# Optimization experiments

Measured on AMD Instinct MI355X. Metric: run time of the kernel, lower is better.

The kernel has to match this reference:

```python
import jax, jax.numpy as jnp
import numpy as np

IN_DIM, OUT_DIM, ATTN_DIM, N_REL = 128, 128, 64, 200
N_NODE, N_EDGE, N_QUERY = 50000, 500000, 64
VOCAB = 2 * N_REL + 1  # 401


def setup_inputs() -> dict:
    key = jax.random.key(0)
    ks = jax.random.split(key, 16)
    # edge table [E,7]: col0=r_idx, col2=rel, col4=sub, col5=obj, col6=time; cols 1,3 unused
    e = np.zeros((N_EDGE, 7), dtype=np.int64)
    e[:, 0] = np.asarray(jax.random.randint(ks[0], (N_EDGE,), 0, N_QUERY))
    e[:, 2] = np.asarray(jax.random.randint(ks[1], (N_EDGE,), 0, VOCAB))
    e[:, 4] = np.asarray(jax.random.randint(ks[2], (N_EDGE,), 0, N_NODE))
    e[:, 5] = np.asarray(jax.random.randint(ks[3], (N_EDGE,), 0, N_NODE))
    e[:, 6] = np.asarray(jax.random.randint(ks[4], (N_EDGE,), 0, 1000))
    s = 0.05
    return {
        "q_sub": jax.random.randint(ks[5], (N_QUERY,), 0, N_NODE),
        "q_rel": jax.random.randint(ks[6], (N_QUERY,), 0, VOCAB),
        "hidden": jax.random.normal(ks[7], (N_NODE, IN_DIM), jnp.float32),
        "edges": jnp.asarray(e),
        "n_node": N_NODE,
        "rela_embed": jax.random.normal(ks[8], (VOCAB, IN_DIM), jnp.float32),
        "Ws_W": jax.random.normal(ks[9], (ATTN_DIM, IN_DIM), jnp.float32) * s,
        "Wr_W": jax.random.normal(ks[10], (ATTN_DIM, IN_DIM), jnp.float32) * s,
        "Wqr_W": jax.random.normal(ks[11], (ATTN_DIM, IN_DIM), jnp.float32) * s,
        "Wqr_b": jnp.zeros((ATTN_DIM,), jnp.float32),
        "walpha_W": jax.random.normal(ks[12], (1, ATTN_DIM), jnp.float32) * s,
        "gateW_W": jax.random.normal(ks[13], (2 * IN_DIM, 3 * IN_DIM), jnp.float32) * s,
        "gateW_b": jnp.zeros((2 * IN_DIM,), jnp.float32),
        "ht_W": jax.random.normal(ks[14], (IN_DIM, 2 * IN_DIM), jnp.float32) * s,
        "ht_b": jnp.zeros((IN_DIM,), jnp.float32),
        "Wh_W": jax.random.normal(ks[15], (OUT_DIM, IN_DIM), jnp.float32) * s,
    }


def reference(q_sub, q_rel, hidden, edges, n_node, rela_embed,
              Ws_W, Wr_W, Wqr_W, Wqr_b, walpha_W,
              gateW_W, gateW_b, ht_W, ht_b, Wh_W):
    sub, rel, obj, r_idx = edges[:, 4], edges[:, 2], edges[:, 5], edges[:, 0]
    # unique+inverse on (rel,time) then embedding of rel == direct embedding lookup
    hr = rela_embed[rel]              # [E, in]
    hs = hidden[sub]                  # [E, in]
    h_qr = rela_embed[q_rel][r_idx]   # [E, in]
    # GateUnit(message=hr, factor=h_qr, hidden_state=hs)
    factors = jnp.concatenate([hr, h_qr, hs], axis=1)
    gates = jax.nn.sigmoid(factors @ gateW_W.T + gateW_b)
    update, reset = jnp.split(gates, 2, axis=1)
    cand = jnp.tanh(jnp.concatenate([hr, reset * hs], axis=1) @ ht_W.T + ht_b)
    message = (1.0 - update) * hs + update * cand
    # attention score
    pre = hs @ Ws_W.T + hr @ Wr_W.T + (h_qr @ Wqr_W.T + Wqr_b)
    alpha = jax.nn.leaky_relu(pre, 0.01) @ walpha_W.T  # [E,1]
    up_message = jax.nn.sigmoid(alpha) * message
    # scatter-sum over destination nodes + sqrt-degree normalization
    agg = jax.ops.segment_sum(up_message, obj, num_segments=n_node)
    deg = jax.ops.segment_sum(jnp.ones((up_message.shape[0], 1), jnp.float32), obj, num_segments=n_node)
    agg = agg / jnp.sqrt(deg + 0.0001)
    return agg @ Wh_W.T  # act = identity
```

## Files before the change

kernel.cpp:

```cpp
#include <hip/hip_runtime.h>

typedef unsigned short ushort_t;
typedef __attribute__((ext_vector_type(8))) short short8;
typedef __attribute__((ext_vector_type(4))) float f32x4;

#define DEV __device__ __forceinline__

DEV float sigm(float x) { return 1.0f / (1.0f + __expf(-x)); }
DEV float tanh_fast(float x) { return 1.0f - 2.0f / (__expf(2.0f * x) + 1.0f); }
DEV ushort_t f2bf(float v) {
    unsigned u = __float_as_uint(v);
    unsigned r = (u + 0x7fffu + ((u >> 16) & 1u)) >> 16;
    return (ushort_t)r;
}
DEV float bf2f(ushort_t h) { return __uint_as_float(((unsigned)h) << 16); }
DEV unsigned cvt_pk(float lo, float hi) {
    unsigned r;
    asm("v_cvt_pk_bf16_f32 %0, %1, %2" : "=v"(r) : "v"(lo), "v"(hi));
    return r;
}
DEV float dot4(float4 a, float4 b) {
    return fmaf(a.x, b.x, fmaf(a.y, b.y, fmaf(a.z, b.z, a.w * b.w)));
}

__global__ __launch_bounds__(256) void hist_kernel(
    const int* __restrict__ edges, int nEdge, int* __restrict__ cnt)
{
    int i = blockIdx.x * 256 + threadIdx.x;
    if (i < nEdge) atomicAdd(cnt + edges[(size_t)i * 7 + 5], 1);
}

__global__ __launch_bounds__(256) void scan1_kernel(
    const int* __restrict__ cnt, int n, int* __restrict__ partials)
{
    __shared__ int s[256];
    int t = threadIdx.x;
    int i = blockIdx.x * 256 + t;
    s[t] = (i < n) ? cnt[i] : 0;
    __syncthreads();
    for (int o = 128; o > 0; o >>= 1) {
        if (t < o) s[t] += s[t + o];
        __syncthreads();
    }
    if (t == 0) partials[blockIdx.x] = s[0];
}

__global__ __launch_bounds__(256) void scan2_kernel(
    const int* __restrict__ cnt, int n, const int* __restrict__ partials,
    int nBlk, int* __restrict__ start, int* __restrict__ cursor)
{
    __shared__ int ps[256];
    __shared__ int loc[256];
    int t = threadIdx.x, b = blockIdx.x;
    ps[t] = (t < nBlk) ? partials[t] : 0;
    __syncthreads();
    for (int o = 1; o < 256; o <<= 1) {
        int v = (t >= o) ? ps[t - o] : 0;
        __syncthreads();
        ps[t] += v;
        __syncthreads();
    }
    int offset = (b > 0) ? ps[b - 1] : 0;
    int i = b * 256 + t;
    int v = (i < n) ? cnt[i] : 0;
    loc[t] = v;
    __syncthreads();
    for (int o = 1; o < 256; o <<= 1) {
        int x = (t >= o) ? loc[t - o] : 0;
        __syncthreads();
        loc[t] += x;
        __syncthreads();
    }
    if (i < n) {
        int excl = offset + loc[t] - v;
        start[i] = excl;
        cursor[i] = excl;
    }
}

__global__ __launch_bounds__(256) void build_kernel(
    const int* __restrict__ edges, int nEdge, int* __restrict__ cursor,
    int4* __restrict__ sorted)
{
    int i = blockIdx.x * 256 + threadIdx.x;
    if (i < nEdge) {
        const int* er = edges + (size_t)i * 7;
        int obj = er[5];
        int s = atomicAdd(cursor + obj, 1);
        sorted[s] = make_int4(er[0], er[2], er[4], obj);
    }
}

__global__ __launch_bounds__(256) void table_kernel(
    const float* __restrict__ rela, const int* __restrict__ q_rel,
    const float* __restrict__ gateW, const float* __restrict__ gateW_b,
    const float* __restrict__ WrW, const float* __restrict__ WqrW,
    const float* __restrict__ Wqr_b, const float* __restrict__ htW,
    const float* __restrict__ ht_b,
    float* __restrict__ grhr, float* __restrict__ gq,
    float* __restrict__ whr, float* __restrict__ wq,
    float* __restrict__ thr, int vocab)
{
    __shared__ float x[128];
    int b = blockIdx.x, t = threadIdx.x;
    bool isRel = b < vocab;
    int src = isRel ? b : q_rel[b - vocab];
    if (t < 128) x[t] = rela[src * 128 + t];
    __syncthreads();
    const float4* x4 = (const float4*)x;
    {
        const float4* wrow = (const float4*)(gateW + t * 384 + (isRel ? 0 : 128));
        float acc = isRel ? 0.0f : gateW_b[t];
#pragma unroll 8
        for (int i = 0; i < 32; i++) acc += dot4(wrow[i], x4[i]);
        float* dst = isRel ? (grhr + b * 256) : (gq + (b - vocab) * 256);
        dst[2 * (t & 127) + (t >> 7)] = acc;
    }
    if (isRel) {
        if (t < 192) {
            bool isWr = t < 64;
            int i = isWr ? t : (t - 64);
            const float4* wrow = (const float4*)(isWr ? (WrW + i * 128) : (htW + i * 256));
            float acc = isWr ? 0.0f : ht_b[i];
#pragma unroll 8
            for (int q = 0; q < 32; q++) acc += dot4(wrow[q], x4[q]);
            if (isWr) whr[b * 64 + i] = acc;
            else      thr[b * 128 + i] = acc;
        }
    } else {
        if (t < 64) {
            const float4* wrow = (const float4*)(WqrW + t * 128);
            float acc = Wqr_b[t];
#pragma unroll 8
            for (int q = 0; q < 32; q++) acc += dot4(wrow[q], x4[q]);
            wq[(b - vocab) * 64 + t] = acc;
        }
    }
}

__global__ __launch_bounds__(256) void node_kernel(
    const float* __restrict__ hidden, const float* __restrict__ gateW,
    const float* __restrict__ WsW,
    ushort_t* __restrict__ gate_hs, ushort_t* __restrict__ ws_hs,
    ushort_t* __restrict__ hsb, int nNode)
{
    __shared__ char a_lds[32 * 256];
    int t = threadIdx.x, w = t >> 6, l = t & 63;
    int lm = l & 15, lh = l >> 4;
    int nbase = blockIdx.x * 32;

    for (int idx = t; idx < 1024; idx += 256) {
        int row = idx >> 5, c4 = idx & 31;
        int node = nbase + row;
        float4 v = (node < nNode) ? ((const float4*)hidden)[(size_t)node * 32 + c4]
                                  : float4{0.f, 0.f, 0.f, 0.f};
        uint2 p;
        p.x = cvt_pk(v.x, v.y);
        p.y = cvt_pk(v.z, v.w);
        *(uint2*)(a_lds + ((row * 256 + c4 * 8) ^ ((row & 7) << 4))) = p;
        if (node < nNode) *(uint2*)(hsb + (size_t)node * 128 + c4 * 4) = p;
    }

    short8 bfr[5][4];
#pragma unroll
    for (int nt = 0; nt < 5; nt++)
#pragma unroll
        for (int kt = 0; kt < 4; kt++) {
            int row = w * 80 + nt * 16 + lm;
            const float* src = (row < 256)
                ? gateW + (size_t)row * 384 + 256 + kt * 32 + lh * 8
                : WsW + (size_t)(row - 256) * 128 + kt * 32 + lh * 8;
            float4 f0 = *(const float4*)src;
            float4 f1 = *(const float4*)(src + 4);
            union { unsigned u[4]; short8 s; } tmp;
            tmp.u[0] = cvt_pk(f0.x, f0.y); tmp.u[1] = cvt_pk(f0.z, f0.w);
            tmp.u[2] = cvt_pk(f1.x, f1.y); tmp.u[3] = cvt_pk(f1.z, f1.w);
            bfr[nt][kt] = tmp.s;
        }
    __syncthreads();

    short8 afr[2][4];
#pragma unroll
    for (int mt = 0; mt < 2; mt++)
#pragma unroll
        for (int kt = 0; kt < 4; kt++) {
            int row = mt * 16 + lm;
            afr[mt][kt] = *(const short8*)(a_lds +
                ((row * 256 + kt * 64 + lh * 16) ^ ((row & 7) << 4)));
        }
    f32x4 acc[2][5];
#pragma unroll
    for (int mt = 0; mt < 2; mt++)
#pragma unroll
        for (int nt = 0; nt < 5; nt++) acc[mt][nt] = (f32x4){0.f, 0.f, 0.f, 0.f};
#pragma unroll
    for (int kt = 0; kt < 4; kt++)
#pragma unroll
        for (int mt = 0; mt < 2; mt++)
#pragma unroll
            for (int nt = 0; nt < 5; nt++)
                acc[mt][nt] = __builtin_amdgcn_mfma_f32_16x16x32_bf16(
                    afr[mt][kt], bfr[nt][kt], acc[mt][nt], 0, 0, 0);

#pragma unroll
    for (int mt = 0; mt < 2; mt++)
#pragma unroll
        for (int nt = 0; nt < 5; nt++) {
            int wrow = w * 80 + nt * 16 + lm;
#pragma unroll
            for (int r = 0; r < 4; r++) {
                int node = nbase + mt * 16 + lh * 4 + r;
                if (node < nNode) {
                    ushort_t v = f2bf(acc[mt][nt][r]);
                    if (wrow < 256)
                        gate_hs[(size_t)node * 256 + 2 * (wrow & 127) + (wrow >> 7)] = v;
                    else
                        ws_hs[(size_t)node * 64 + wrow - 256] = v;
                }
            }
        }
}

__global__ __launch_bounds__(256, 6) void edge_kernel(
    const int4* __restrict__ sorted, int nEdge,
    const float* __restrict__ grhr, const float* __restrict__ gq,
    const float* __restrict__ whr, const float* __restrict__ wq,
    const float* __restrict__ thr,
    const ushort_t* __restrict__ gate_hs, const ushort_t* __restrict__ ws_hs,
    const ushort_t* __restrict__ hsb,
    const float* __restrict__ walpha, const float* __restrict__ htW,
    float* __restrict__ agg)
{
    __shared__ ushort_t xb[32 * 128];
    __shared__ unsigned ab[32 * 128];
    __shared__ int4 eds4[32];

    int t = threadIdx.x, w = t >> 6, l = t & 63;
    int lm = l & 15, lh = l >> 4;
    int n0 = w * 32;

    int nb = gridDim.x;
    int xcd = blockIdx.x & 7, lid = blockIdx.x >> 3;
    int q = nb >> 3, rr = nb & 7;
    int sbid = ((xcd < rr) ? xcd * (q + 1) : rr * (q + 1) + (xcd - rr) * q) + lid;
    int ebase = sbid * 32;

    if (t < 32) {
        int gi = ebase + t;
        eds4[t] = (gi < nEdge) ? sorted[gi] : make_int4(0, 0, 0, -1);
    }

    short8 bfr[2][4];
#pragma unroll
    for (int nt = 0; nt < 2; nt++)
#pragma unroll
        for (int kt = 0; kt < 4; kt++) {
            const float* src = htW + (size_t)(n0 + nt * 16 + lm) * 256 + 128 + kt * 32 + lh * 8;
            float4 f0 = *(const float4*)src;
            float4 f1 = *(const float4*)(src + 4);
            union { unsigned u[4]; short8 s; } tmp;
            tmp.u[0] = cvt_pk(f0.x, f0.y); tmp.u[1] = cvt_pk(f0.z, f0.w);
            tmp.u[2] = cvt_pk(f1.x, f1.y); tmp.u[3] = cvt_pk(f1.z, f1.w);
            bfr[nt][kt] = tmp.s;
        }
    float wal = walpha[l];
    __syncthreads();

#pragma unroll 4
    for (int i = 0; i < 8; i++) {
        int e = w * 8 + i;
        int4 er = eds4[e];
        int ridx = er.x, rel = er.y, sub = er.z;
        ushort4 gp = *(const ushort4*)(gate_hs + (size_t)sub * 256 + 4 * l);
        float4 ga = *(const float4*)(grhr + (size_t)rel * 256 + 4 * l);
        float4 gb = *(const float4*)(gq + (size_t)ridx * 256 + 4 * l);
        unsigned hp = *(const unsigned*)(hsb + (size_t)sub * 128 + 2 * l);
        float h0 = bf2f((ushort_t)(hp & 0xffffu));
        float h1 = bf2f((ushort_t)(hp >> 16));
        float u0 = sigm(ga.x + gb.x + bf2f(gp.x));
        float r0 = sigm(ga.y + gb.y + bf2f(gp.y));
        float u1 = sigm(ga.z + gb.z + bf2f(gp.z));
        float r1 = sigm(ga.w + gb.w + bf2f(gp.w));
        float aa = bf2f(ws_hs[(size_t)sub * 64 + l]) + whr[rel * 64 + l] + wq[ridx * 64 + l];
        aa = (aa > 0.0f) ? aa : 0.01f * aa;
        float v = aa * wal;
#pragma unroll
        for (int o = 32; o > 0; o >>= 1) v += __shfl_xor(v, o, 64);
        float sga = sigm(v);
        unsigned xw = cvt_pk(r0 * h0, r1 * h1);
        *(unsigned*)((char*)xb + ((e * 256 + 4 * l) ^ ((e & 7) << 4))) = xw;
        float A0 = sga * (1.0f - u0) * h0;
        float A1 = sga * (1.0f - u1) * h1;
        uint2 abp;
        abp.x = cvt_pk(A0, sga * u0);
        abp.y = cvt_pk(A1, sga * u1);
        *(uint2*)((char*)ab + ((e * 512 + 8 * l) ^ (((e >> 2) & 3) << 6))) = abp;
    }
    __syncthreads();

    short8 afr[2][4];
#pragma unroll
    for (int mt = 0; mt < 2; mt++)
#pragma unroll
        for (int kt = 0; kt < 4; kt++) {
            int e = mt * 16 + lm;
            afr[mt][kt] = *(const short8*)((const char*)xb +
                ((e * 256 + kt * 64 + lh * 16) ^ ((e & 7) << 4)));
        }
    f32x4 acc[2][2];
#pragma unroll
    for (int mt = 0; mt < 2; mt++)
#pragma unroll
        for (int nt = 0; nt < 2; nt++) acc[mt][nt] = (f32x4){0.f, 0.f, 0.f, 0.f};
#pragma unroll
    for (int kt = 0; kt < 4; kt++)
#pragma unroll
        for (int mt = 0; mt < 2; mt++)
#pragma unroll
            for (int nt = 0; nt < 2; nt++)
                acc[mt][nt] = __builtin_amdgcn_mfma_f32_16x16x32_bf16(
                    afr[mt][kt], bfr[nt][kt], acc[mt][nt], 0, 0, 0);

#pragma unroll
    for (int mt = 0; mt < 2; mt++)
#pragma unroll
        for (int nt = 0; nt < 2; nt++) {
            int d = n0 + nt * 16 + lm;
            float vals[4];
            int objs[4];
#pragma unroll
            for (int r = 0; r < 4; r++) {
                int e = mt * 16 + lh * 4 + r;
                int rel = eds4[e].y;
                objs[r] = eds4[e].w;
                float th = thr[rel * 128 + d];
                float cand = tanh_fast(acc[mt][nt][r] + th);
                unsigned abw = *(const unsigned*)((const char*)ab +
                    ((e * 512 + 4 * d) ^ (((e >> 2) & 3) << 6)));
                vals[r] = bf2f((ushort_t)(abw & 0xffffu)) +
                          bf2f((ushort_t)(abw >> 16)) * cand;
            }
            float sum = vals[0];
            int prev = objs[0];
#pragma unroll
            for (int r = 1; r < 4; r++) {
                if (objs[r] == prev) {
                    sum += vals[r];
                } else {
                    if (prev >= 0) atomicAdd(agg + (size_t)prev * 128 + d, sum);
                    sum = vals[r];
                    prev = objs[r];
                }
            }
            if (prev >= 0) atomicAdd(agg + (size_t)prev * 128 + d, sum);
        }
}

__global__ __launch_bounds__(256) void final_kernel(
    const float* __restrict__ WhW, const int* __restrict__ degi,
    float* __restrict__ agg, int nNode)
{
    __shared__ char y_lds[64 * 256];
    int t = threadIdx.x, w = t >> 6, l = t & 63;
    int lm = l & 15, lh = l >> 4;
    int nbase = blockIdx.x * 64;

    short8 bfr[2][4];
#pragma unroll
    for (int nt = 0; nt < 2; nt++)
#pragma unroll
        for (int kt = 0; kt < 4; kt++) {
            const float* src = WhW + (size_t)(w * 32 + nt * 16 + lm) * 128 + kt * 32 + lh * 8;
            float4 f0 = *(const float4*)src;
            float4 f1 = *(const float4*)(src + 4);
            union { unsigned u[4]; short8 s; } tmp;
            tmp.u[0] = cvt_pk(f0.x, f0.y); tmp.u[1] = cvt_pk(f0.z, f0.w);
            tmp.u[2] = cvt_pk(f1.x, f1.y); tmp.u[3] = cvt_pk(f1.z, f1.w);
            bfr[nt][kt] = tmp.s;
        }

    for (int idx = t; idx < 2048; idx += 256) {
        int row = idx >> 5, c4 = idx & 31;
        int node = nbase + row;
        uint2 p = {0u, 0u};
        if (node < nNode) {
            float4 v = ((const float4*)agg)[(size_t)node * 32 + c4];
            float r = 1.0f / sqrtf((float)degi[node] + 1e-4f);
            p.x = cvt_pk(v.x * r, v.y * r);
            p.y = cvt_pk(v.z * r, v.w * r);
        }
        *(uint2*)(y_lds + ((row * 256 + c4 * 8) ^ ((row & 7) << 4))) = p;
    }
    __syncthreads();

    short8 afr[4][4];
#pragma unroll
    for (int mt = 0; mt < 4; mt++)
#pragma unroll
        for (int kt = 0; kt < 4; kt++) {
            int row = mt * 16 + lm;
            afr[mt][kt] = *(const short8*)(y_lds +
                ((row * 256 + kt * 64 + lh * 16) ^ ((row & 7) << 4)));
        }
    f32x4 acc[4][2];
#pragma unroll
    for (int mt = 0; mt < 4; mt++)
#pragma unroll
        for (int nt = 0; nt < 2; nt++) acc[mt][nt] = (f32x4){0.f, 0.f, 0.f, 0.f};
#pragma unroll
    for (int kt = 0; kt < 4; kt++)
#pragma unroll
        for (int mt = 0; mt < 4; mt++)
#pragma unroll
            for (int nt = 0; nt < 2; nt++)
                acc[mt][nt] = __builtin_amdgcn_mfma_f32_16x16x32_bf16(
                    afr[mt][kt], bfr[nt][kt], acc[mt][nt], 0, 0, 0);

#pragma unroll
    for (int mt = 0; mt < 4; mt++)
#pragma unroll
        for (int nt = 0; nt < 2; nt++) {
            int col = w * 32 + nt * 16 + lm;
#pragma unroll
            for (int r = 0; r < 4; r++) {
                int node = nbase + mt * 16 + lh * 4 + r;
                if (node < nNode) agg[(size_t)node * 128 + col] = acc[mt][nt][r];
            }
        }
}

extern "C" void kernel_launch(void* const* d_in, const int* in_sizes, int n_in,
                              void* d_out, int out_size, void* d_ws, size_t ws_size,
                              hipStream_t stream)
{
    const int*   q_rel   = (const int*)d_in[1];
    const float* hidden  = (const float*)d_in[2];
    const int*   edges   = (const int*)d_in[3];
    const float* rela    = (const float*)d_in[5];
    const float* WsW     = (const float*)d_in[6];
    const float* WrW     = (const float*)d_in[7];
    const float* WqrW    = (const float*)d_in[8];
    const float* Wqr_b   = (const float*)d_in[9];
    const float* walpha  = (const float*)d_in[10];
    const float* gateW   = (const float*)d_in[11];
    const float* gateW_b = (const float*)d_in[12];
    const float* htW     = (const float*)d_in[13];
    const float* ht_b    = (const float*)d_in[14];
    const float* WhW     = (const float*)d_in[15];

    int nNode  = in_sizes[2] / 128;
    int nEdge  = in_sizes[3] / 7;
    int vocab  = in_sizes[5] / 128;
    int nQuery = in_sizes[1];

    char* ws = (char*)d_ws;
    size_t off = 0;
    auto alloc = [&](size_t bytes) { size_t o = off; off += (bytes + 255) & ~(size_t)255; return o; };
    int*      cntO    = (int*)(ws + alloc((size_t)(nNode + 256) * 4));
    int*      startO  = (int*)(ws + alloc((size_t)(nNode + 256) * 4));
    int*      cursorO = (int*)(ws + alloc((size_t)(nNode + 256) * 4));
    int*      partials= (int*)(ws + alloc(256 * 4));
    int4*     sorted  = (int4*)(ws + alloc((size_t)nEdge * 16));
    float*    grhr    = (float*)(ws + alloc((size_t)vocab * 256 * 4));
    float*    whr     = (float*)(ws + alloc((size_t)vocab * 64 * 4));
    float*    thr     = (float*)(ws + alloc((size_t)vocab * 128 * 4));
    float*    gq      = (float*)(ws + alloc((size_t)nQuery * 256 * 4));
    float*    wq      = (float*)(ws + alloc((size_t)nQuery * 64 * 4));
    ushort_t* gate_hs = (ushort_t*)(ws + alloc((size_t)nNode * 256 * 2));
    ushort_t* ws_hs   = (ushort_t*)(ws + alloc((size_t)nNode * 64 * 2));
    ushort_t* hsb     = (ushort_t*)(ws + alloc((size_t)nNode * 128 * 2));
    if (off > ws_size) return;

    float* agg = (float*)d_out;
    hipMemsetAsync(agg, 0, (size_t)nNode * 128 * 4, stream);
    hipMemsetAsync(cntO, 0, (size_t)(nNode + 256) * 4, stream);

    hist_kernel<<<(nEdge + 255) / 256, 256, 0, stream>>>(edges, nEdge, cntO);
    int nScan = nNode + 1;
    int nBlk = (nScan + 255) / 256;
    scan1_kernel<<<nBlk, 256, 0, stream>>>(cntO, nScan, partials);
    scan2_kernel<<<nBlk, 256, 0, stream>>>(cntO, nScan, partials, nBlk, startO, cursorO);
    build_kernel<<<(nEdge + 255) / 256, 256, 0, stream>>>(edges, nEdge, cursorO, sorted);

    table_kernel<<<vocab + nQuery, 256, 0, stream>>>(
        rela, q_rel, gateW, gateW_b, WrW, WqrW, Wqr_b, htW, ht_b,
        grhr, gq, whr, wq, thr, vocab);

    int ngrp = (nNode + 31) / 32;
    node_kernel<<<ngrp, 256, 0, stream>>>(hidden, gateW, WsW, gate_hs, ws_hs, hsb, nNode);

    int eblocks = (nEdge + 31) / 32;
    edge_kernel<<<eblocks, 256, 0, stream>>>(
        sorted, nEdge, grhr, gq, whr, wq, thr,
        gate_hs, ws_hs, hsb, walpha, htW, agg);

    int fblocks = (nNode + 63) / 64;
    final_kernel<<<fblocks, 256, 0, stream>>>(WhW, cntO, agg, nNode);
}
```

Baseline: 448.4 us.

## Merge node, table and histogram kernels; batch attention reductions in edge kernel

The node projection, relation table and degree histogram kernels become one launch that dispatches on block index ranges, which cuts launch overhead and lets the independent stages run concurrently. In the edge kernel, the eight per-edge attention shuffle reductions are batched so they interleave, and the sigmoid attention weight is kept in shared memory and applied after the MFMA rather than folded into the bf16 coefficients. The MFMA accumulators are also seeded with the thr bias before the matmul. Risks are extra register pressure from holding eight partial sums plus a small numerical change from storing the unscaled coefficients in bf16.

```diff
diff --git a/kernel.cpp b/kernel.cpp
--- a/kernel.cpp
+++ b/kernel.cpp
@@ -23,11 +23,141 @@
     return fmaf(a.x, b.x, fmaf(a.y, b.y, fmaf(a.z, b.z, a.w * b.w)));
 }
 
-__global__ __launch_bounds__(256) void hist_kernel(
-    const int* __restrict__ edges, int nEdge, int* __restrict__ cnt)
-{
-    int i = blockIdx.x * 256 + threadIdx.x;
-    if (i < nEdge) atomicAdd(cnt + edges[(size_t)i * 7 + 5], 1);
+__global__ __launch_bounds__(256) void prep_kernel(
+    const float* __restrict__ hidden, const float* __restrict__ gateW,
+    const float* __restrict__ WsW,
+    ushort_t* __restrict__ gate_hs, ushort_t* __restrict__ ws_hs,
+    ushort_t* __restrict__ hsb, int nNode,
+    const float* __restrict__ rela, const int* __restrict__ q_rel,
+    const float* __restrict__ gateW_b,
+    const float* __restrict__ WrW, const float* __restrict__ WqrW,
+    const float* __restrict__ Wqr_b, const float* __restrict__ htW,
+    const float* __restrict__ ht_b,
+    float* __restrict__ grhr, float* __restrict__ gq,
+    float* __restrict__ whr, float* __restrict__ wq,
+    float* __restrict__ thr, int vocab,
+    const int* __restrict__ edges, int nEdge, int* __restrict__ cnt,
+    int nodeB, int tableB)
+{
+    __shared__ char smem[8192];
+    int bid = blockIdx.x, t = threadIdx.x;
+
+    if (bid < nodeB) {
+        char* a_lds = smem;
+        int w = t >> 6, l = t & 63;
+        int lm = l & 15, lh = l >> 4;
+        int nbase = bid * 32;
+
+        for (int idx = t; idx < 1024; idx += 256) {
+            int row = idx >> 5, c4 = idx & 31;
+            int node = nbase + row;
+            float4 v = (node < nNode) ? ((const float4*)hidden)[(size_t)node * 32 + c4]
+                                      : float4{0.f, 0.f, 0.f, 0.f};
+            uint2 p;
+            p.x = cvt_pk(v.x, v.y);
+            p.y = cvt_pk(v.z, v.w);
+            *(uint2*)(a_lds + ((row * 256 + c4 * 8) ^ ((row & 7) << 4))) = p;
+            if (node < nNode) *(uint2*)(hsb + (size_t)node * 128 + c4 * 4) = p;
+        }
+
+        short8 bfr[5][4];
+#pragma unroll
+        for (int nt = 0; nt < 5; nt++)
+#pragma unroll
+            for (int kt = 0; kt < 4; kt++) {
+                int row = w * 80 + nt * 16 + lm;
+                const float* src = (row < 256)
+                    ? gateW + (size_t)row * 384 + 256 + kt * 32 + lh * 8
+                    : WsW + (size_t)(row - 256) * 128 + kt * 32 + lh * 8;
+                float4 f0 = *(const float4*)src;
+                float4 f1 = *(const float4*)(src + 4);
+                union { unsigned u[4]; short8 s; } tmp;
+                tmp.u[0] = cvt_pk(f0.x, f0.y); tmp.u[1] = cvt_pk(f0.z, f0.w);
+                tmp.u[2] = cvt_pk(f1.x, f1.y); tmp.u[3] = cvt_pk(f1.z, f1.w);
+                bfr[nt][kt] = tmp.s;
+            }
+        __syncthreads();
+
+        short8 afr[2][4];
+#pragma unroll
+        for (int mt = 0; mt < 2; mt++)
+#pragma unroll
+            for (int kt = 0; kt < 4; kt++) {
+                int row = mt * 16 + lm;
+                afr[mt][kt] = *(const short8*)(a_lds +
+                    ((row * 256 + kt * 64 + lh * 16) ^ ((row & 7) << 4)));
+            }
+        f32x4 acc[2][5];
+#pragma unroll
+        for (int mt = 0; mt < 2; mt++)
+#pragma unroll
+            for (int nt = 0; nt < 5; nt++) acc[mt][nt] = (f32x4){0.f, 0.f, 0.f, 0.f};
+#pragma unroll
+        for (int kt = 0; kt < 4; kt++)
+#pragma unroll
+            for (int mt = 0; mt < 2; mt++)
+#pragma unroll
+                for (int nt = 0; nt < 5; nt++)
+                    acc[mt][nt] = __builtin_amdgcn_mfma_f32_16x16x32_bf16(
+                        afr[mt][kt], bfr[nt][kt], acc[mt][nt], 0, 0, 0);
+
+#pragma unroll
+        for (int mt = 0; mt < 2; mt++)
+#pragma unroll
+            for (int nt = 0; nt < 5; nt++) {
+                int wrow = w * 80 + nt * 16 + lm;
+#pragma unroll
+                for (int r = 0; r < 4; r++) {
+                    int node = nbase + mt * 16 + lh * 4 + r;
+                    if (node < nNode) {
+                        ushort_t v = f2bf(acc[mt][nt][r]);
+                        if (wrow < 256)
+                            gate_hs[(size_t)node * 256 + 2 * (wrow & 127) + (wrow >> 7)] = v;
+                        else
+                            ws_hs[(size_t)node * 64 + wrow - 256] = v;
+                    }
+                }
+            }
+    } else if (bid < nodeB + tableB) {
+        float* x = (float*)smem;
+        int b = bid - nodeB;
+        bool isRel = b < vocab;
+        int src = isRel ? b : q_rel[b - vocab];
+        if (t < 128) x[t] = rela[src * 128 + t];
+        __syncthreads();
+        const float4* x4 = (const float4*)x;
+        {
+            const float4* wrow = (const float4*)(gateW + t * 384 + (isRel ? 0 : 128));
+            float acc = isRel ? 0.0f : gateW_b[t];
+#pragma unroll 8
+            for (int i = 0; i < 32; i++) acc += dot4(wrow[i], x4[i]);
+            float* dst = isRel ? (grhr + b * 256) : (gq + (b - vocab) * 256);
+            dst[2 * (t & 127) + (t >> 7)] = acc;
+        }
+        if (isRel) {
+            if (t < 192) {
+                bool isWr = t < 64;
+                int i = isWr ? t : (t - 64);
+                const float4* wrow = (const float4*)(isWr ? (WrW + i * 128) : (htW + i * 256));
+                float acc = isWr ? 0.0f : ht_b[i];
+#pragma unroll 8
+                for (int q = 0; q < 32; q++) acc += dot4(wrow[q], x4[q]);
+                if (isWr) whr[b * 64 + i] = acc;
+                else      thr[b * 128 + i] = acc;
+            }
+        } else {
+            if (t < 64) {
+                const float4* wrow = (const float4*)(WqrW + t * 128);
+                float acc = Wqr_b[t];
+#pragma unroll 8
+                for (int q = 0; q < 32; q++) acc += dot4(wrow[q], x4[q]);
+                wq[(b - vocab) * 64 + t] = acc;
+            }
+        }
+    } else {
+        int i = (bid - nodeB - tableB) * 256 + t;
+        if (i < nEdge) atomicAdd(cnt + edges[(size_t)i * 7 + 5], 1);
+    }
 }
 
 __global__ __launch_bounds__(256) void scan1_kernel(
@@ -89,136 +219,6 @@
         int s = atomicAdd(cursor + obj, 1);
         sorted[s] = make_int4(er[0], er[2], er[4], obj);
     }
-}
-
-__global__ __launch_bounds__(256) void table_kernel(
-    const float* __restrict__ rela, const int* __restrict__ q_rel,
-    const float* __restrict__ gateW, const float* __restrict__ gateW_b,
-    const float* __restrict__ WrW, const float* __restrict__ WqrW,
-    const float* __restrict__ Wqr_b, const float* __restrict__ htW,
-    const float* __restrict__ ht_b,
-    float* __restrict__ grhr, float* __restrict__ gq,
-    float* __restrict__ whr, float* __restrict__ wq,
-    float* __restrict__ thr, int vocab)
-{
-    __shared__ float x[128];
-    int b = blockIdx.x, t = threadIdx.x;
-    bool isRel = b < vocab;
-    int src = isRel ? b : q_rel[b - vocab];
-    if (t < 128) x[t] = rela[src * 128 + t];
-    __syncthreads();
-    const float4* x4 = (const float4*)x;
-    {
-        const float4* wrow = (const float4*)(gateW + t * 384 + (isRel ? 0 : 128));
-        float acc = isRel ? 0.0f : gateW_b[t];
-#pragma unroll 8
-        for (int i = 0; i < 32; i++) acc += dot4(wrow[i], x4[i]);
-        float* dst = isRel ? (grhr + b * 256) : (gq + (b - vocab) * 256);
-        dst[2 * (t & 127) + (t >> 7)] = acc;
-    }
-    if (isRel) {
-        if (t < 192) {
-            bool isWr = t < 64;
-            int i = isWr ? t : (t - 64);
-            const float4* wrow = (const float4*)(isWr ? (WrW + i * 128) : (htW + i * 256));
-            float acc = isWr ? 0.0f : ht_b[i];
-#pragma unroll 8
-            for (int q = 0; q < 32; q++) acc += dot4(wrow[q], x4[q]);
-            if (isWr) whr[b * 64 + i] = acc;
-            else      thr[b * 128 + i] = acc;
-        }
-    } else {
-        if (t < 64) {
-            const float4* wrow = (const float4*)(WqrW + t * 128);
-            float acc = Wqr_b[t];
-#pragma unroll 8
-            for (int q = 0; q < 32; q++) acc += dot4(wrow[q], x4[q]);
-            wq[(b - vocab) * 64 + t] = acc;
-        }
-    }
-}
-
-__global__ __launch_bounds__(256) void node_kernel(
-    const float* __restrict__ hidden, const float* __restrict__ gateW,
-    const float* __restrict__ WsW,
-    ushort_t* __restrict__ gate_hs, ushort_t* __restrict__ ws_hs,
-    ushort_t* __restrict__ hsb, int nNode)
-{
-    __shared__ char a_lds[32 * 256];
-    int t = threadIdx.x, w = t >> 6, l = t & 63;
-    int lm = l & 15, lh = l >> 4;
-    int nbase = blockIdx.x * 32;
-
-    for (int idx = t; idx < 1024; idx += 256) {
-        int row = idx >> 5, c4 = idx & 31;
-        int node = nbase + row;
-        float4 v = (node < nNode) ? ((const float4*)hidden)[(size_t)node * 32 + c4]
-                                  : float4{0.f, 0.f, 0.f, 0.f};
-        uint2 p;
-        p.x = cvt_pk(v.x, v.y);
-        p.y = cvt_pk(v.z, v.w);
-        *(uint2*)(a_lds + ((row * 256 + c4 * 8) ^ ((row & 7) << 4))) = p;
-        if (node < nNode) *(uint2*)(hsb + (size_t)node * 128 + c4 * 4) = p;
-    }
-
-    short8 bfr[5][4];
-#pragma unroll
-    for (int nt = 0; nt < 5; nt++)
-#pragma unroll
-        for (int kt = 0; kt < 4; kt++) {
-            int row = w * 80 + nt * 16 + lm;
-            const float* src = (row < 256)
-                ? gateW + (size_t)row * 384 + 256 + kt * 32 + lh * 8
-                : WsW + (size_t)(row - 256) * 128 + kt * 32 + lh * 8;
-            float4 f0 = *(const float4*)src;
-            float4 f1 = *(const float4*)(src + 4);
-            union { unsigned u[4]; short8 s; } tmp;
-            tmp.u[0] = cvt_pk(f0.x, f0.y); tmp.u[1] = cvt_pk(f0.z, f0.w);
-            tmp.u[2] = cvt_pk(f1.x, f1.y); tmp.u[3] = cvt_pk(f1.z, f1.w);
-            bfr[nt][kt] = tmp.s;
-        }
-    __syncthreads();
-
-    short8 afr[2][4];
-#pragma unroll
-    for (int mt = 0; mt < 2; mt++)
-#pragma unroll
-        for (int kt = 0; kt < 4; kt++) {
-            int row = mt * 16 + lm;
-            afr[mt][kt] = *(const short8*)(a_lds +
-                ((row * 256 + kt * 64 + lh * 16) ^ ((row & 7) << 4)));
-        }
-    f32x4 acc[2][5];
-#pragma unroll
-    for (int mt = 0; mt < 2; mt++)
-#pragma unroll
-        for (int nt = 0; nt < 5; nt++) acc[mt][nt] = (f32x4){0.f, 0.f, 0.f, 0.f};
-#pragma unroll
-    for (int kt = 0; kt < 4; kt++)
-#pragma unroll
-        for (int mt = 0; mt < 2; mt++)
-#pragma unroll
-            for (int nt = 0; nt < 5; nt++)
-                acc[mt][nt] = __builtin_amdgcn_mfma_f32_16x16x32_bf16(
-                    afr[mt][kt], bfr[nt][kt], acc[mt][nt], 0, 0, 0);
-
-#pragma unroll
-    for (int mt = 0; mt < 2; mt++)
-#pragma unroll
-        for (int nt = 0; nt < 5; nt++) {
-            int wrow = w * 80 + nt * 16 + lm;
-#pragma unroll
-            for (int r = 0; r < 4; r++) {
-                int node = nbase + mt * 16 + lh * 4 + r;
-                if (node < nNode) {
-                    ushort_t v = f2bf(acc[mt][nt][r]);
-                    if (wrow < 256)
-                        gate_hs[(size_t)node * 256 + 2 * (wrow & 127) + (wrow >> 7)] = v;
-                    else
-                        ws_hs[(size_t)node * 64 + wrow - 256] = v;
-                }
-            }
-        }
 }
 
 __global__ __launch_bounds__(256, 6) void edge_kernel(
@@ -233,6 +233,7 @@
 {
     __shared__ ushort_t xb[32 * 128];
     __shared__ unsigned ab[32 * 128];
+    __shared__ float sgaL[32];
     __shared__ int4 eds4[32];
 
     int t = threadIdx.x, w = t >> 6, l = t & 63;
@@ -266,7 +267,8 @@
     float wal = walpha[l];
     __syncthreads();
 
-#pragma unroll 4
+    float aa8[8];
+#pragma unroll
     for (int i = 0; i < 8; i++) {
         int e = w * 8 + i;
         int4 er = eds4[e];
@@ -275,26 +277,44 @@
         float4 ga = *(const float4*)(grhr + (size_t)rel * 256 + 4 * l);
         float4 gb = *(const float4*)(gq + (size_t)ridx * 256 + 4 * l);
         unsigned hp = *(const unsigned*)(hsb + (size_t)sub * 128 + 2 * l);
+        float aw = bf2f(ws_hs[(size_t)sub * 64 + l]) + whr[rel * 64 + l] + wq[ridx * 64 + l];
         float h0 = bf2f((ushort_t)(hp & 0xffffu));
         float h1 = bf2f((ushort_t)(hp >> 16));
         float u0 = sigm(ga.x + gb.x + bf2f(gp.x));
         float r0 = sigm(ga.y + gb.y + bf2f(gp.y));
         float u1 = sigm(ga.z + gb.z + bf2f(gp.z));
         float r1 = sigm(ga.w + gb.w + bf2f(gp.w));
-        float aa = bf2f(ws_hs[(size_t)sub * 64 + l]) + whr[rel * 64 + l] + wq[ridx * 64 + l];
-        aa = (aa > 0.0f) ? aa : 0.01f * aa;
-        float v = aa * wal;
-#pragma unroll
-        for (int o = 32; o > 0; o >>= 1) v += __shfl_xor(v, o, 64);
-        float sga = sigm(v);
-        unsigned xw = cvt_pk(r0 * h0, r1 * h1);
-        *(unsigned*)((char*)xb + ((e * 256 + 4 * l) ^ ((e & 7) << 4))) = xw;
-        float A0 = sga * (1.0f - u0) * h0;
-        float A1 = sga * (1.0f - u1) * h1;
+        *(unsigned*)((char*)xb + ((e * 256 + 4 * l) ^ ((e & 7) << 4))) = cvt_pk(r0 * h0, r1 * h1);
         uint2 abp;
-        abp.x = cvt_pk(A0, sga * u0);
-        abp.y = cvt_pk(A1, sga * u1);
+        abp.x = cvt_pk((1.0f - u0) * h0, u0);
+        abp.y = cvt_pk((1.0f - u1) * h1, u1);
         *(uint2*)((char*)ab + ((e * 512 + 8 * l) ^ (((e >> 2) & 3) << 6))) = abp;
+        aw = (aw > 0.0f) ? aw : 0.01f * aw;
+        aa8[i] = aw * wal;
+    }
+
+    f32x4 acc[2][2];
+#pragma unroll
+    for (int mt = 0; mt < 2; mt++)
+#pragma unroll
+        for (int nt = 0; nt < 2; nt++) {
+            int d = n0 + nt * 16 + lm;
+#pragma unroll
+            for (int r = 0; r < 4; r++) {
+                int rel = eds4[mt * 16 + lh * 4 + r].y;
+                acc[mt][nt][r] = thr[rel * 128 + d];
+            }
+        }
+
+#pragma unroll
+    for (int o = 32; o > 0; o >>= 1) {
+#pragma unroll
+        for (int i = 0; i < 8; i++) aa8[i] += __shfl_xor(aa8[i], o, 64);
+    }
+#pragma unroll
+    for (int i = 0; i < 8; i++) {
+        float s = sigm(aa8[i]);
+        if (l == i) sgaL[w * 8 + i] = s;
     }
     __syncthreads();
 
@@ -307,11 +327,6 @@
             afr[mt][kt] = *(const short8*)((const char*)xb +
                 ((e * 256 + kt * 64 + lh * 16) ^ ((e & 7) << 4)));
         }
-    f32x4 acc[2][2];
-#pragma unroll
-    for (int mt = 0; mt < 2; mt++)
-#pragma unroll
-        for (int nt = 0; nt < 2; nt++) acc[mt][nt] = (f32x4){0.f, 0.f, 0.f, 0.f};
 #pragma unroll
     for (int kt = 0; kt < 4; kt++)
 #pragma unroll
@@ -331,14 +346,13 @@
 #pragma unroll
             for (int r = 0; r < 4; r++) {
                 int e = mt * 16 + lh * 4 + r;
-                int rel = eds4[e].y;
                 objs[r] = eds4[e].w;
-                float th = thr[rel * 128 + d];
-                float cand = tanh_fast(acc[mt][nt][r] + th);
+                float cand = tanh_fast(acc[mt][nt][r]);
                 unsigned abw = *(const unsigned*)((const char*)ab +
                     ((e * 512 + 4 * d) ^ (((e >> 2) & 3) << 6)));
-                vals[r] = bf2f((ushort_t)(abw & 0xffffu)) +
-                          bf2f((ushort_t)(abw >> 16)) * cand;
+                float sg = sgaL[e];
+                vals[r] = sg * (bf2f((ushort_t)(abw & 0xffffu)) +
+                                bf2f((ushort_t)(abw >> 16)) * cand);
             }
             float sum = vals[0];
             int prev = objs[0];
@@ -475,20 +489,21 @@
     hipMemsetAsync(agg, 0, (size_t)nNode * 128 * 4, stream);
     hipMemsetAsync(cntO, 0, (size_t)(nNode + 256) * 4, stream);
 
-    hist_kernel<<<(nEdge + 255) / 256, 256, 0, stream>>>(edges, nEdge, cntO);
+    int nodeB  = (nNode + 31) / 32;
+    int tableB = vocab + nQuery;
+    int histB  = (nEdge + 255) / 256;
+    prep_kernel<<<nodeB + tableB + histB, 256, 0, stream>>>(
+        hidden, gateW, WsW, gate_hs, ws_hs, hsb, nNode,
+        rela, q_rel, gateW_b, WrW, WqrW, Wqr_b, htW, ht_b,
+        grhr, gq, whr, wq, thr, vocab,
+        edges, nEdge, cntO, nodeB, tableB);
+
     int nScan = nNode + 1;
     int nBlk = (nScan + 255) / 256;
     scan1_kernel<<<nBlk, 256, 0, stream>>>(cntO, nScan, partials);
     scan2_kernel<<<nBlk, 256, 0, stream>>>(cntO, nScan, partials, nBlk, startO, cursorO);
     build_kernel<<<(nEdge + 255) / 256, 256, 0, stream>>>(edges, nEdge, cursorO, sorted);
 
-    table_kernel<<<vocab + nQuery, 256, 0, stream>>>(
-        rela, q_rel, gateW, gateW_b, WrW, WqrW, Wqr_b, htW, ht_b,
-        grhr, gq, whr, wq, thr, vocab);
-
-    int ngrp = (nNode + 31) / 32;
-    node_kernel<<<ngrp, 256, 0, stream>>>(hidden, gateW, WsW, gate_hs, ws_hs, hsb, nNode);
-
     int eblocks = (nEdge + 31) / 32;
     edge_kernel<<<eblocks, 256, 0, stream>>>(
         sorted, nEdge, grhr, gq, whr, wq, thr,
```

Result: faster. 375.6 us (-16.2%).
